# Optimization experiments

Hardware: AMD Instinct MI355X
Metric: run time of the kernel (lower is better)

Reference implementation:

```python
import jax, jax.numpy as jnp
import numpy as np

NZ, NC = 100, 2
FEAT_NUMBER, FEATURE_DIM = 8192, 1024
B = 8192
BN_EPS = 1e-5
GUMBEL_EPS = 0.001
TEMP = 0.1


def _batchnorm(h, gamma, beta):
    # torch BatchNorm1d training mode: biased batch statistics
    mu = jnp.mean(h, axis=0, keepdims=True)
    var = jnp.var(h, axis=0, keepdims=True)
    return (h - mu) * jax.lax.rsqrt(var + BN_EPS) * gamma + beta


def setup_inputs() -> dict:
    key = jax.random.key(0)
    ks = jax.random.split(key, 16)
    def glorot(k, shape):
        lim = 1.0 / np.sqrt(shape[0])
        return jax.random.uniform(k, shape, jnp.float32, -lim, lim)
    return {
        "x": jax.random.normal(ks[0], (B, NZ), jnp.float32),
        "y": jax.random.uniform(ks[1], (B, NC), jnp.float32),
        "W1": glorot(ks[2], (NZ + NC, 256)), "b1": jnp.zeros((256,), jnp.float32),
        "g1": jnp.ones((256,), jnp.float32), "be1": jnp.zeros((256,), jnp.float32),
        "W2": glorot(ks[3], (256, 64)), "b2": jnp.zeros((64,), jnp.float32),
        "g2": jnp.ones((64,), jnp.float32), "be2": jnp.zeros((64,), jnp.float32),
        "W3": glorot(ks[4], (64, FEAT_NUMBER)), "b3": jnp.zeros((FEAT_NUMBER,), jnp.float32),
        "codebook": jax.random.normal(ks[5], (FEAT_NUMBER, FEATURE_DIM), jnp.float32),
    }


def reference(x, y, W1, b1, g1, be1, W2, b2, g2, be2, W3, b3, codebook):
    z = jnp.concatenate([x, y], axis=-1)                       # [B, nz+nc]
    h = jax.nn.relu(_batchnorm(z @ W1 + b1, g1, be1))          # [B, 256]
    h = jax.nn.relu(_batchnorm(h @ W2 + b2, g2, be2))          # [B, 64]
    logits = h @ W3 + b3                                       # [B, feat_number]

    # gumbel noise: U = eps*rand; g = -log(-log(U+eps)+eps)
    U = GUMBEL_EPS * jax.random.uniform(jax.random.key(42), logits.shape, jnp.float32)
    g = -jnp.log(-jnp.log(U + GUMBEL_EPS) + GUMBEL_EPS)
    y_soft = jax.nn.softmax((logits + g) / TEMP, axis=-1)

    # straight-through one-hot
    ind = jnp.argmax(y_soft, axis=-1)
    y_hard = jax.nn.one_hot(ind, FEAT_NUMBER, dtype=y_soft.dtype)
    z_st = jax.lax.stop_gradient(y_hard - y_soft) + y_soft     # [B, feat_number]

    # weighted codebook sum == matmul (avoids [B,F,D] broadcast intermediate)
    return jnp.einsum('bf,fd->bd', z_st, codebook)             # [B, feature_dim]
```

## Files before the change

### kernel.cpp

```cpp
#include <hip/hip_runtime.h>
#include <math.h>

#define B_ROWS   8192
#define NZ       100
#define NC       2
#define H1       256
#define H2       64
#define FEATN    8192
#define FDIM     1024
#define RROWS    16
#define NTILE    (FEATN / 16)
#define A1ROWS   16
#define A1BLKS   (B_ROWS / A1ROWS)
#define CONVBLKS 256
#define A2ROWS   16
#define A2BLKS   (B_ROWS / A2ROWS)

typedef __attribute__((ext_vector_type(8))) short short8;
typedef __attribute__((ext_vector_type(4))) float f32x4;

__device__ __forceinline__ unsigned rotl32(unsigned v, int r) {
    return (v << r) | (v >> (32 - r));
}
__device__ __forceinline__ unsigned threefry_bits(unsigned lo) {
    const unsigned ks0 = 0u, ks1 = 42u, ks2 = 0x1BD11BDAu ^ 42u;
    unsigned x0 = 0u + ks0;
    unsigned x1 = lo + ks1;
#define TF_R4(a,b,c,d) \
    x0 += x1; x1 = rotl32(x1,a); x1 ^= x0; \
    x0 += x1; x1 = rotl32(x1,b); x1 ^= x0; \
    x0 += x1; x1 = rotl32(x1,c); x1 ^= x0; \
    x0 += x1; x1 = rotl32(x1,d); x1 ^= x0;
    TF_R4(13,15,26,6);  x0 += ks1; x1 += ks2 + 1u;
    TF_R4(17,29,16,24); x0 += ks2; x1 += ks0 + 2u;
    TF_R4(13,15,26,6);  x0 += ks0; x1 += ks1 + 3u;
    TF_R4(17,29,16,24); x0 += ks1; x1 += ks2 + 4u;
    TF_R4(13,15,26,6);  x0 += ks2; x1 += ks0 + 5u;
#undef TF_R4
    return x0 ^ x1;
}
__device__ __forceinline__ float gumbel_g(unsigned flat) {
    unsigned bits = threefry_bits(flat);
    float u  = __uint_as_float((bits >> 9) | 0x3f800000u) - 1.0f;
    float U  = 0.001f * u;
    float t1 = U + 0.001f;
    float L1 = (float)log((double)t1);
    float A  = 0.001f - L1;
    float L2 = (float)log((double)A);
    return -L2;
}

__device__ __forceinline__ unsigned short f2bf(float x) {
    unsigned u = __float_as_uint(x);
    u += 0x7fffu + ((u >> 16) & 1u);
    return (unsigned short)(u >> 16);
}
__device__ __forceinline__ unsigned fmono(float x) {
    unsigned b = __float_as_uint(x);
    return (b & 0x80000000u) ? ~b : (b | 0x80000000u);
}

__global__ __launch_bounds__(256) void k_a1(
    const float* __restrict__ x, const float* __restrict__ y,
    const float* __restrict__ W1, const float* __restrict__ b1,
    const float* __restrict__ W3,
    float* __restrict__ a1, double* __restrict__ p1, double* __restrict__ p2,
    unsigned short* __restrict__ w3s, float* __restrict__ maxw)
{
    const int t = threadIdx.x;

    if (blockIdx.x >= A1BLKS) {
        const int job  = (blockIdx.x - A1BLKS) * 256 + t;
        const int T    = job >> 7;
        const int rem  = job & 127;
        const int kh   = rem >> 6;
        const int l    = rem & 63;
        const int quad = l >> 4, col = l & 15;
        const float* src = W3 + (size_t)(kh * 32 + quad * 8) * FEATN + T * 16 + col;
        unsigned short v[8];
        float mx = 0.0f;
#pragma unroll
        for (int jj = 0; jj < 8; ++jj) {
            float xv = src[(size_t)jj * FEATN];
            mx = fmaxf(mx, fabsf(xv));
            v[jj] = f2bf(xv);
        }
        uint4 o;
        o.x = (unsigned)v[0] | ((unsigned)v[1] << 16);
        o.y = (unsigned)v[2] | ((unsigned)v[3] << 16);
        o.z = (unsigned)v[4] | ((unsigned)v[5] << 16);
        o.w = (unsigned)v[6] | ((unsigned)v[7] << 16);
        ((uint4*)w3s)[job] = o;
#pragma unroll
        for (int off = 32; off; off >>= 1) mx = fmaxf(mx, __shfl_xor(mx, off));
        __shared__ float wred[4];
        if ((t & 63) == 0) wred[t >> 6] = mx;
        __syncthreads();
        if (t == 0) {
            float m = fmaxf(fmaxf(wred[0], wred[1]), fmaxf(wred[2], wred[3]));
            atomicMax((unsigned*)maxw, __float_as_uint(m));
        }
        return;
    }

    const int j  = t;
    const int b0 = blockIdx.x * A1ROWS;

    __shared__ __align__(16) float xs[NZ][16];
    __shared__ __align__(16) float ys[NC][16];
    for (int q = t; q < A1ROWS * NZ; q += 256) {
        int r = q / NZ, i = q - r * NZ;
        xs[i][r] = x[(size_t)b0 * NZ + q];
    }
    if (t < A1ROWS * NC) {
        int r = t >> 1, i = t & 1;
        ys[i][r] = y[b0 * NC + t];
    }
    __syncthreads();

    double acc[A1ROWS];
#pragma unroll
    for (int r = 0; r < A1ROWS; ++r) acc[r] = 0.0;
    for (int i = 0; i < NZ; ++i) {
        double wd = (double)W1[i * H1 + j];
        const float4 x0 = *(const float4*)&xs[i][0];
        const float4 x1 = *(const float4*)&xs[i][4];
        const float4 x2 = *(const float4*)&xs[i][8];
        const float4 x3 = *(const float4*)&xs[i][12];
        acc[0]  += (double)x0.x * wd; acc[1]  += (double)x0.y * wd;
        acc[2]  += (double)x0.z * wd; acc[3]  += (double)x0.w * wd;
        acc[4]  += (double)x1.x * wd; acc[5]  += (double)x1.y * wd;
        acc[6]  += (double)x1.z * wd; acc[7]  += (double)x1.w * wd;
        acc[8]  += (double)x2.x * wd; acc[9]  += (double)x2.y * wd;
        acc[10] += (double)x2.z * wd; acc[11] += (double)x2.w * wd;
        acc[12] += (double)x3.x * wd; acc[13] += (double)x3.y * wd;
        acc[14] += (double)x3.z * wd; acc[15] += (double)x3.w * wd;
    }
#pragma unroll
    for (int i = 0; i < NC; ++i) {
        double wd = (double)W1[(NZ + i) * H1 + j];
        const float4 y0 = *(const float4*)&ys[i][0];
        const float4 y1 = *(const float4*)&ys[i][4];
        const float4 y2 = *(const float4*)&ys[i][8];
        const float4 y3 = *(const float4*)&ys[i][12];
        acc[0]  += (double)y0.x * wd; acc[1]  += (double)y0.y * wd;
        acc[2]  += (double)y0.z * wd; acc[3]  += (double)y0.w * wd;
        acc[4]  += (double)y1.x * wd; acc[5]  += (double)y1.y * wd;
        acc[6]  += (double)y1.z * wd; acc[7]  += (double)y1.w * wd;
        acc[8]  += (double)y2.x * wd; acc[9]  += (double)y2.y * wd;
        acc[10] += (double)y2.z * wd; acc[11] += (double)y2.w * wd;
        acc[12] += (double)y3.x * wd; acc[13] += (double)y3.y * wd;
        acc[14] += (double)y3.z * wd; acc[15] += (double)y3.w * wd;
    }
    double bb = (double)b1[j];
    double s = 0.0, s2 = 0.0;
#pragma unroll
    for (int r = 0; r < A1ROWS; ++r) {
        float v = (float)(acc[r] + bb);
        a1[(b0 + r) * H1 + j] = v;
        double dv = (double)v;
        s += dv; s2 += dv * dv;
    }
    p1[blockIdx.x * H1 + j] = s;
    p2[blockIdx.x * H1 + j] = s2;
}

__global__ __launch_bounds__(256) void k_stats2(
    const double* __restrict__ p1, const double* __restrict__ p2,
    int nprt, int ncol,
    const float* __restrict__ gamma, const float* __restrict__ beta,
    float* __restrict__ scale, float* __restrict__ shift)
{
    const int j = blockIdx.x, t = threadIdx.x;
    double s = 0.0, s2 = 0.0;
    for (int g = t; g < nprt; g += 256) {
        s  += p1[(size_t)g * ncol + j];
        s2 += p2[(size_t)g * ncol + j];
    }
#pragma unroll
    for (int off = 32; off; off >>= 1) {
        s  += __shfl_xor(s, off);
        s2 += __shfl_xor(s2, off);
    }
    __shared__ double ws1[4], ws2[4];
    if ((t & 63) == 0) { ws1[t >> 6] = s; ws2[t >> 6] = s2; }
    __syncthreads();
    if (t == 0) {
        s  = (ws1[0] + ws1[1]) + (ws1[2] + ws1[3]);
        s2 = (ws2[0] + ws2[1]) + (ws2[2] + ws2[3]);
        double mean = s * (1.0 / B_ROWS);
        double var  = s2 * (1.0 / B_ROWS) - mean * mean;
        double rstd = 1.0 / sqrt(var + 1e-5);
        double sc   = (double)gamma[j] * rstd;
        scale[j] = (float)sc;
        shift[j] = (float)((double)beta[j] - mean * sc);
    }
}

__global__ __launch_bounds__(256) void k_a2(
    const float* __restrict__ a1,
    const float* __restrict__ sc1, const float* __restrict__ sh1,
    const float* __restrict__ W2, const float* __restrict__ b2,
    float* __restrict__ a2, double* __restrict__ p1, double* __restrict__ p2)
{
    const int t  = threadIdx.x;
    const int k  = t & 63;
    const int rg = t >> 6;
    const int b0 = blockIdx.x * A2ROWS;

    __shared__ __align__(16) float hs[H1][20];
    __shared__ double ps[4][64], ps2[4][64];

    {
        const float sct = sc1[t], sht = sh1[t];
#pragma unroll 4
        for (int rr = 0; rr < A2ROWS; ++rr) {
            float v = a1[(size_t)(b0 + rr) * H1 + t];
            hs[t][rr] = fmaxf(fmaf(v, sct, sht), 0.0f);
        }
    }
    __syncthreads();

    const int r0 = rg * 4;
    double acc0 = 0.0, acc1 = 0.0, acc2 = 0.0, acc3 = 0.0;
    for (int j = 0; j < H1; ++j) {
        double wd = (double)W2[j * H2 + k];
        const float4 h4 = *(const float4*)&hs[j][r0];
        acc0 += (double)h4.x * wd;
        acc1 += (double)h4.y * wd;
        acc2 += (double)h4.z * wd;
        acc3 += (double)h4.w * wd;
    }
    const double bb = (double)b2[k];
    float v0 = (float)(acc0 + bb);
    float v1 = (float)(acc1 + bb);
    float v2 = (float)(acc2 + bb);
    float v3 = (float)(acc3 + bb);
    a2[(b0 + r0 + 0) * H2 + k] = v0;
    a2[(b0 + r0 + 1) * H2 + k] = v1;
    a2[(b0 + r0 + 2) * H2 + k] = v2;
    a2[(b0 + r0 + 3) * H2 + k] = v3;

    double s  = (double)v0 + (double)v1 + (double)v2 + (double)v3;
    double s2 = (double)v0 * (double)v0 + (double)v1 * (double)v1
              + (double)v2 * (double)v2 + (double)v3 * (double)v3;
    ps[rg][k] = s; ps2[rg][k] = s2;
    __syncthreads();
    if (t < 64) {
        double S  = (ps[0][t]  + ps[1][t])  + (ps[2][t]  + ps[3][t]);
        double S2 = (ps2[0][t] + ps2[1][t]) + (ps2[2][t] + ps2[3][t]);
        p1[blockIdx.x * H2 + t] = S;
        p2[blockIdx.x * H2 + t] = S2;
    }
}

__global__ __launch_bounds__(512)
__attribute__((amdgpu_waves_per_eu(4, 4)))
void k_main(
    const float* __restrict__ a2,
    const float* __restrict__ sc2, const float* __restrict__ sh2,
    const float* __restrict__ W3, const float* __restrict__ b3,
    const unsigned short* __restrict__ w3s, const float* __restrict__ maxw,
    const float* __restrict__ codebook, float* __restrict__ out)
{
    const int t    = threadIdx.x;
    const int wv   = t >> 6;
    const int lane = t & 63;
    const int quad = lane >> 4, col = lane & 15;
    const int b0   = blockIdx.x * RROWS;

    __shared__ __align__(16) float h2T[64][17];
    __shared__ float fineT[NTILE][17];
    __shared__ float thrS[RROWS];
    __shared__ unsigned long long best[RROWS];
    __shared__ unsigned short wl[RROWS * NTILE];
    __shared__ int wlN;
    __shared__ int rowInd[RROWS];
    __shared__ float maxwS;

    if (t == 0) { maxwS = maxw[0]; wlN = 0; }
    for (int q = t; q < RROWS * 64; q += 512) {
        int j = q >> 4, r = q & 15;
        float v = a2[(b0 + r) * H2 + j];
        h2T[j][r] = fmaxf(fmaf(v, sc2[j], sh2[j]), 0.0f);
    }
    __syncthreads();

    short8 aF0, aF1;
#pragma unroll
    for (int jj = 0; jj < 8; ++jj) {
        aF0[jj] = (short)f2bf(h2T[quad * 8 + jj][col]);
        aF1[jj] = (short)f2bf(h2T[32 + quad * 8 + jj][col]);
    }

    {
        const uint4*  wp = (const uint4*)w3s + (size_t)wv * 8192 + lane;
        const float4* bq = (const float4*)b3 + wv * 256 + quad;
        for (int s = 0; s < 8; ++s) {
            uint4 c[8], d[8];
            float4 bb[8];
#pragma unroll
            for (int u = 0; u < 8; ++u) {
                c[u]  = wp[u * 128];
                d[u]  = wp[u * 128 + 64];
                bb[u] = bq[u * 4];
            }
#pragma unroll
            for (int u = 0; u < 8; ++u) {
                f32x4 acc = {bb[u].x, bb[u].y, bb[u].z, bb[u].w};
                acc = __builtin_amdgcn_mfma_f32_16x16x32_bf16(
                          *(const short8*)&c[u], aF0, acc, 0, 0, 0);
                acc = __builtin_amdgcn_mfma_f32_16x16x32_bf16(
                          *(const short8*)&d[u], aF1, acc, 0, 0, 0);
                float m = fmaxf(fmaxf(acc[0], acc[1]), fmaxf(acc[2], acc[3]));
                m = fmaxf(m, __shfl_xor(m, 16));
                m = fmaxf(m, __shfl_xor(m, 32));
                if (lane < 16) fineT[(wv * 8 + s) * 8 + u][lane] = m;
            }
            wp += 1024; bq += 32;
        }
    }
    __syncthreads();

    {
        const int r = t >> 5, cc = t & 31;
        float s = fabsf(h2T[2 * cc][r]) + fabsf(h2T[2 * cc + 1][r]);
        float gmv = -1e30f;
#pragma unroll
        for (int k = 0; k < 16; ++k) gmv = fmaxf(gmv, fineT[cc + 32 * k][r]);
#pragma unroll
        for (int off = 1; off < 32; off <<= 1) {
            s   += __shfl_xor(s, off);
            gmv  = fmaxf(gmv, __shfl_xor(gmv, off));
        }
        if (cc == 0) {
            float e = s * maxwS * (1.0f / 256.0f);
            thrS[r] = gmv - (0.1068f + e + 1e-3f);
            best[r] = 0ull;
        }
    }
    __syncthreads();

    {
        const int r = t >> 5, cc = t & 31;
        const float th = thrS[r];
#pragma unroll
        for (int k = 0; k < 16; ++k) {
            const int T = cc + 32 * k;
            if (fineT[T][r] >= th) {
                int idx = atomicAdd(&wlN, 1);
                wl[idx] = (unsigned short)((r << 9) | T);
            }
        }
    }
    __syncthreads();

    {
        const int n = wlN;
        const int g = lane >> 4;
        for (int i = wv * 4; i < n; i += 32) {
            const int  ci  = i + g;
            const bool act = (ci < n);
            const int  e   = act ? wl[ci] : 0;
            const int  r   = e >> 9;
            const int  T   = e & 511;
            const int  f   = T * 16 + col;
            float acc = b3[f];
            const float* wcol = W3 + f;
#pragma unroll 8
            for (int j = 0; j < 64; ++j) {
                acc = fmaf(h2T[j][r], *wcol, acc);
                wcol += FEATN;
            }
            if (act && acc >= thrS[r]) {
                float sc = acc + gumbel_g((unsigned)(b0 + r) * (unsigned)FEATN + (unsigned)f);
                unsigned long long pk = ((unsigned long long)fmono(sc) << 32)
                                      | (unsigned)(FEATN - 1 - f);
                atomicMax(&best[r], pk);
            }
        }
    }
    __syncthreads();
    if (t < RROWS) {
        rowInd[t] = (FEATN - 1 - (int)(best[t] & 0xFFFFFFFFull)) & (FEATN - 1);
    }
    __syncthreads();

    {
        const int rr = t >> 8, tt = t & 255;
        for (int rp = 0; rp < RROWS / 2; ++rp) {
            const int r = rp * 2 + rr;
            const int ind = rowInd[r];
            const float4* src = (const float4*)(codebook + (size_t)ind * FDIM);
            float4*       dst = (float4*)(out + (size_t)(b0 + r) * FDIM);
            dst[tt] = src[tt];
        }
    }
}

extern "C" void kernel_launch(void* const* d_in, const int* in_sizes, int n_in,
                              void* d_out, int out_size, void* d_ws, size_t ws_size,
                              hipStream_t stream)
{
    const float* x   = (const float*)d_in[0];
    const float* y   = (const float*)d_in[1];
    const float* W1  = (const float*)d_in[2];
    const float* b1  = (const float*)d_in[3];
    const float* g1  = (const float*)d_in[4];
    const float* be1 = (const float*)d_in[5];
    const float* W2  = (const float*)d_in[6];
    const float* b2  = (const float*)d_in[7];
    const float* g2  = (const float*)d_in[8];
    const float* be2 = (const float*)d_in[9];
    const float* W3  = (const float*)d_in[10];
    const float* b3  = (const float*)d_in[11];
    const float* cb  = (const float*)d_in[12];
    float* out = (float*)d_out;

    float* ws  = (float*)d_ws;
    float* a1  = ws;
    float* a2  = a1 + B_ROWS * H1;
    float* sc1 = a2 + B_ROWS * H2;
    float* sh1 = sc1 + H1;
    float* sc2 = sh1 + H1;
    float* sh2 = sc2 + H2;
    double* p1 = (double*)(sh2 + H2);
    double* p2 = p1 + A1BLKS * H1;
    unsigned short* w3s = (unsigned short*)(p2 + A1BLKS * H1);
    float* maxw = (float*)(w3s + NTILE * 2 * 64 * 8);

    hipMemsetAsync(maxw, 0, 4, stream);
    k_a1    <<<A1BLKS + CONVBLKS, 256, 0, stream>>>(x, y, W1, b1, W3,
                                                    a1, p1, p2, w3s, maxw);
    k_stats2<<<H1, 256, 0, stream>>>(p1, p2, A1BLKS, H1, g1, be1, sc1, sh1);
    k_a2    <<<A2BLKS, 256, 0, stream>>>(a1, sc1, sh1, W2, b2, a2, p1, p2);
    k_stats2<<<H2, 256, 0, stream>>>(p1, p2, A2BLKS, H2, g2, be2, sc2, sh2);
    k_main  <<<B_ROWS / RROWS, 512, 0, stream>>>(a2, sc2, sh2, W3, b3,
                                                 w3s, maxw, cb, out);
}
```

Baseline: 214.5 us.

## Split feature dimension across two blocks per row group and move codebook gather to separate kernel

The main kernel now processes half the feature tiles per block and launches twice as many blocks. Per-row argmax is combined through global 64-bit atomicMax into a buffer that reuses the a1 workspace, and a new kernel then gathers codebook rows. The per-tile maxima are stored as bf16 rounded upward, with the threshold margin widened to match, which halves the shared memory used for them. Occupancy is raised to 8 waves per EU, and the small MLP kernels move to 512-thread blocks. The cost is an extra memset and an extra launch, global atomics, and the threshold-based pruning depending on the bf16 rounding staying conservative.

```diff
diff --git a/kernel.cpp b/kernel.cpp
--- a/kernel.cpp
+++ b/kernel.cpp
@@ -10,9 +10,10 @@
 #define FDIM     1024
 #define RROWS    16
 #define NTILE    (FEATN / 16)
+#define NTILE_H  (NTILE / 2)
 #define A1ROWS   16
 #define A1BLKS   (B_ROWS / A1ROWS)
-#define CONVBLKS 256
+#define CONVBLKS 128
 #define A2ROWS   16
 #define A2BLKS   (B_ROWS / A2ROWS)
 
@@ -55,12 +56,20 @@
     u += 0x7fffu + ((u >> 16) & 1u);
     return (unsigned short)(u >> 16);
 }
+__device__ __forceinline__ unsigned short f2bf_up(float x) {
+    unsigned u = __float_as_uint(x);
+    unsigned hi = (u & 0x80000000u) ? (u >> 16) : ((u + 0xFFFFu) >> 16);
+    return (unsigned short)hi;
+}
+__device__ __forceinline__ float bf2f(unsigned short h) {
+    return __uint_as_float((unsigned)h << 16);
+}
 __device__ __forceinline__ unsigned fmono(float x) {
     unsigned b = __float_as_uint(x);
     return (b & 0x80000000u) ? ~b : (b | 0x80000000u);
 }
 
-__global__ __launch_bounds__(256) void k_a1(
+__global__ __launch_bounds__(512) void k_a1(
     const float* __restrict__ x, const float* __restrict__ y,
     const float* __restrict__ W1, const float* __restrict__ b1,
     const float* __restrict__ W3,
@@ -70,7 +79,7 @@
     const int t = threadIdx.x;
 
     if (blockIdx.x >= A1BLKS) {
-        const int job  = (blockIdx.x - A1BLKS) * 256 + t;
+        const int job  = (blockIdx.x - A1BLKS) * 512 + t;
         const int T    = job >> 7;
         const int rem  = job & 127;
         const int kh   = rem >> 6;
@@ -93,22 +102,27 @@
         ((uint4*)w3s)[job] = o;
 #pragma unroll
         for (int off = 32; off; off >>= 1) mx = fmaxf(mx, __shfl_xor(mx, off));
-        __shared__ float wred[4];
+        __shared__ float wred[8];
         if ((t & 63) == 0) wred[t >> 6] = mx;
         __syncthreads();
         if (t == 0) {
-            float m = fmaxf(fmaxf(wred[0], wred[1]), fmaxf(wred[2], wred[3]));
+            float m = wred[0];
+#pragma unroll
+            for (int wq = 1; wq < 8; ++wq) m = fmaxf(m, wred[wq]);
             atomicMax((unsigned*)maxw, __float_as_uint(m));
         }
         return;
     }
 
-    const int j  = t;
-    const int b0 = blockIdx.x * A1ROWS;
+    const int j    = t & 255;
+    const int half = t >> 8;
+    const int b0   = blockIdx.x * A1ROWS;
+    const int r0   = half * 8;
 
     __shared__ __align__(16) float xs[NZ][16];
     __shared__ __align__(16) float ys[NC][16];
-    for (int q = t; q < A1ROWS * NZ; q += 256) {
+    __shared__ float vsh[256][8];
+    for (int q = t; q < A1ROWS * NZ; q += 512) {
         int r = q / NZ, i = q - r * NZ;
         xs[i][r] = x[(size_t)b0 * NZ + q];
     }
@@ -118,51 +132,55 @@
     }
     __syncthreads();
 
-    double acc[A1ROWS];
-#pragma unroll
-    for (int r = 0; r < A1ROWS; ++r) acc[r] = 0.0;
+    double acc[8];
+#pragma unroll
+    for (int r = 0; r < 8; ++r) acc[r] = 0.0;
     for (int i = 0; i < NZ; ++i) {
         double wd = (double)W1[i * H1 + j];
-        const float4 x0 = *(const float4*)&xs[i][0];
-        const float4 x1 = *(const float4*)&xs[i][4];
-        const float4 x2 = *(const float4*)&xs[i][8];
-        const float4 x3 = *(const float4*)&xs[i][12];
-        acc[0]  += (double)x0.x * wd; acc[1]  += (double)x0.y * wd;
-        acc[2]  += (double)x0.z * wd; acc[3]  += (double)x0.w * wd;
-        acc[4]  += (double)x1.x * wd; acc[5]  += (double)x1.y * wd;
-        acc[6]  += (double)x1.z * wd; acc[7]  += (double)x1.w * wd;
-        acc[8]  += (double)x2.x * wd; acc[9]  += (double)x2.y * wd;
-        acc[10] += (double)x2.z * wd; acc[11] += (double)x2.w * wd;
-        acc[12] += (double)x3.x * wd; acc[13] += (double)x3.y * wd;
-        acc[14] += (double)x3.z * wd; acc[15] += (double)x3.w * wd;
+        const float4 x0 = *(const float4*)&xs[i][r0];
+        const float4 x1 = *(const float4*)&xs[i][r0 + 4];
+        acc[0] += (double)x0.x * wd; acc[1] += (double)x0.y * wd;
+        acc[2] += (double)x0.z * wd; acc[3] += (double)x0.w * wd;
+        acc[4] += (double)x1.x * wd; acc[5] += (double)x1.y * wd;
+        acc[6] += (double)x1.z * wd; acc[7] += (double)x1.w * wd;
     }
 #pragma unroll
     for (int i = 0; i < NC; ++i) {
         double wd = (double)W1[(NZ + i) * H1 + j];
-        const float4 y0 = *(const float4*)&ys[i][0];
-        const float4 y1 = *(const float4*)&ys[i][4];
-        const float4 y2 = *(const float4*)&ys[i][8];
-        const float4 y3 = *(const float4*)&ys[i][12];
-        acc[0]  += (double)y0.x * wd; acc[1]  += (double)y0.y * wd;
-        acc[2]  += (double)y0.z * wd; acc[3]  += (double)y0.w * wd;
-        acc[4]  += (double)y1.x * wd; acc[5]  += (double)y1.y * wd;
-        acc[6]  += (double)y1.z * wd; acc[7]  += (double)y1.w * wd;
-        acc[8]  += (double)y2.x * wd; acc[9]  += (double)y2.y * wd;
-        acc[10] += (double)y2.z * wd; acc[11] += (double)y2.w * wd;
-        acc[12] += (double)y3.x * wd; acc[13] += (double)y3.y * wd;
-        acc[14] += (double)y3.z * wd; acc[15] += (double)y3.w * wd;
-    }
-    double bb = (double)b1[j];
-    double s = 0.0, s2 = 0.0;
-#pragma unroll
-    for (int r = 0; r < A1ROWS; ++r) {
-        float v = (float)(acc[r] + bb);
-        a1[(b0 + r) * H1 + j] = v;
-        double dv = (double)v;
-        s += dv; s2 += dv * dv;
-    }
-    p1[blockIdx.x * H1 + j] = s;
-    p2[blockIdx.x * H1 + j] = s2;
+        const float4 y0 = *(const float4*)&ys[i][r0];
+        const float4 y1 = *(const float4*)&ys[i][r0 + 4];
+        acc[0] += (double)y0.x * wd; acc[1] += (double)y0.y * wd;
+        acc[2] += (double)y0.z * wd; acc[3] += (double)y0.w * wd;
+        acc[4] += (double)y1.x * wd; acc[5] += (double)y1.y * wd;
+        acc[6] += (double)y1.z * wd; acc[7] += (double)y1.w * wd;
+    }
+    const double bb = (double)b1[j];
+    float v[8];
+#pragma unroll
+    for (int r = 0; r < 8; ++r) {
+        v[r] = (float)(acc[r] + bb);
+        a1[(b0 + r0 + r) * H1 + j] = v[r];
+    }
+    if (half) {
+#pragma unroll
+        for (int r = 0; r < 8; ++r) vsh[j][r] = v[r];
+    }
+    __syncthreads();
+    if (!half) {
+        double s = 0.0, s2 = 0.0;
+#pragma unroll
+        for (int r = 0; r < 8; ++r) {
+            double dv = (double)v[r];
+            s += dv; s2 += dv * dv;
+        }
+#pragma unroll
+        for (int r = 0; r < 8; ++r) {
+            double dv = (double)vsh[j][r];
+            s += dv; s2 += dv * dv;
+        }
+        p1[blockIdx.x * H1 + j] = s;
+        p2[blockIdx.x * H1 + j] = s2;
+    }
 }
 
 __global__ __launch_bounds__(256) void k_stats2(
@@ -197,7 +215,7 @@
     }
 }
 
-__global__ __launch_bounds__(256) void k_a2(
+__global__ __launch_bounds__(512) void k_a2(
     const float* __restrict__ a1,
     const float* __restrict__ sc1, const float* __restrict__ sh1,
     const float* __restrict__ W2, const float* __restrict__ b2,
@@ -207,75 +225,71 @@
     const int k  = t & 63;
     const int rg = t >> 6;
     const int b0 = blockIdx.x * A2ROWS;
-
-    __shared__ __align__(16) float hs[H1][20];
-    __shared__ double ps[4][64], ps2[4][64];
+    const int r0 = rg * 2;
+
+    __shared__ __align__(8) float hs[H1][18];
+    __shared__ float vsh[64][17];
 
     {
-        const float sct = sc1[t], sht = sh1[t];
+        const int jc = t & 255, rq = t >> 8;
+        const float sct = sc1[jc], sht = sh1[jc];
+#pragma unroll
+        for (int rr = rq * 8; rr < rq * 8 + 8; ++rr) {
+            float vv = a1[(size_t)(b0 + rr) * H1 + jc];
+            hs[jc][rr] = fmaxf(fmaf(vv, sct, sht), 0.0f);
+        }
+    }
+    __syncthreads();
+
+    double acc0 = 0.0, acc1 = 0.0;
 #pragma unroll 4
-        for (int rr = 0; rr < A2ROWS; ++rr) {
-            float v = a1[(size_t)(b0 + rr) * H1 + t];
-            hs[t][rr] = fmaxf(fmaf(v, sct, sht), 0.0f);
-        }
-    }
-    __syncthreads();
-
-    const int r0 = rg * 4;
-    double acc0 = 0.0, acc1 = 0.0, acc2 = 0.0, acc3 = 0.0;
     for (int j = 0; j < H1; ++j) {
         double wd = (double)W2[j * H2 + k];
-        const float4 h4 = *(const float4*)&hs[j][r0];
-        acc0 += (double)h4.x * wd;
-        acc1 += (double)h4.y * wd;
-        acc2 += (double)h4.z * wd;
-        acc3 += (double)h4.w * wd;
+        const float2 h2 = *(const float2*)&hs[j][r0];
+        acc0 += (double)h2.x * wd;
+        acc1 += (double)h2.y * wd;
     }
     const double bb = (double)b2[k];
     float v0 = (float)(acc0 + bb);
     float v1 = (float)(acc1 + bb);
-    float v2 = (float)(acc2 + bb);
-    float v3 = (float)(acc3 + bb);
     a2[(b0 + r0 + 0) * H2 + k] = v0;
     a2[(b0 + r0 + 1) * H2 + k] = v1;
-    a2[(b0 + r0 + 2) * H2 + k] = v2;
-    a2[(b0 + r0 + 3) * H2 + k] = v3;
-
-    double s  = (double)v0 + (double)v1 + (double)v2 + (double)v3;
-    double s2 = (double)v0 * (double)v0 + (double)v1 * (double)v1
-              + (double)v2 * (double)v2 + (double)v3 * (double)v3;
-    ps[rg][k] = s; ps2[rg][k] = s2;
+    vsh[k][r0]     = v0;
+    vsh[k][r0 + 1] = v1;
     __syncthreads();
     if (t < 64) {
-        double S  = (ps[0][t]  + ps[1][t])  + (ps[2][t]  + ps[3][t]);
-        double S2 = (ps2[0][t] + ps2[1][t]) + (ps2[2][t] + ps2[3][t]);
-        p1[blockIdx.x * H2 + t] = S;
-        p2[blockIdx.x * H2 + t] = S2;
+        double s = 0.0, s2 = 0.0;
+#pragma unroll
+        for (int r = 0; r < A2ROWS; ++r) {
+            double dv = (double)vsh[t][r];
+            s += dv; s2 += dv * dv;
+        }
+        p1[blockIdx.x * H2 + t] = s;
+        p2[blockIdx.x * H2 + t] = s2;
     }
 }
 
 __global__ __launch_bounds__(512)
-__attribute__((amdgpu_waves_per_eu(4, 4)))
+__attribute__((amdgpu_waves_per_eu(8, 8)))
 void k_main(
     const float* __restrict__ a2,
     const float* __restrict__ sc2, const float* __restrict__ sh2,
     const float* __restrict__ W3, const float* __restrict__ b3,
     const unsigned short* __restrict__ w3s, const float* __restrict__ maxw,
-    const float* __restrict__ codebook, float* __restrict__ out)
+    unsigned long long* __restrict__ bestG)
 {
     const int t    = threadIdx.x;
     const int wv   = t >> 6;
     const int lane = t & 63;
     const int quad = lane >> 4, col = lane & 15;
-    const int b0   = blockIdx.x * RROWS;
+    const int half = blockIdx.x & 1;
+    const int b0   = (blockIdx.x >> 1) * RROWS;
 
     __shared__ __align__(16) float h2T[64][17];
-    __shared__ float fineT[NTILE][17];
+    __shared__ unsigned short fineW[NTILE_H][17];
     __shared__ float thrS[RROWS];
-    __shared__ unsigned long long best[RROWS];
-    __shared__ unsigned short wl[RROWS * NTILE];
+    __shared__ unsigned short wl[RROWS * NTILE_H];
     __shared__ int wlN;
-    __shared__ int rowInd[RROWS];
     __shared__ float maxwS;
 
     if (t == 0) { maxwS = maxw[0]; wlN = 0; }
@@ -294,9 +308,10 @@
     }
 
     {
-        const uint4*  wp = (const uint4*)w3s + (size_t)wv * 8192 + lane;
-        const float4* bq = (const float4*)b3 + wv * 256 + quad;
-        for (int s = 0; s < 8; ++s) {
+        const uint4*  wp = (const uint4*)w3s
+                         + (size_t)(half * NTILE_H + wv * 32) * 128 + lane;
+        const float4* bq = (const float4*)b3 + (half * 1024 + wv * 128) + quad;
+        for (int s = 0; s < 4; ++s) {
             uint4 c[8], d[8];
             float4 bb[8];
 #pragma unroll
@@ -315,7 +330,7 @@
                 float m = fmaxf(fmaxf(acc[0], acc[1]), fmaxf(acc[2], acc[3]));
                 m = fmaxf(m, __shfl_xor(m, 16));
                 m = fmaxf(m, __shfl_xor(m, 32));
-                if (lane < 16) fineT[(wv * 8 + s) * 8 + u][lane] = m;
+                if (lane < 16) fineW[wv * 32 + s * 8 + u][lane] = f2bf_up(m);
             }
             wp += 1024; bq += 32;
         }
@@ -327,7 +342,7 @@
         float s = fabsf(h2T[2 * cc][r]) + fabsf(h2T[2 * cc + 1][r]);
         float gmv = -1e30f;
 #pragma unroll
-        for (int k = 0; k < 16; ++k) gmv = fmaxf(gmv, fineT[cc + 32 * k][r]);
+        for (int k = 0; k < 8; ++k) gmv = fmaxf(gmv, bf2f(fineW[cc + 32 * k][r]));
 #pragma unroll
         for (int off = 1; off < 32; off <<= 1) {
             s   += __shfl_xor(s, off);
@@ -335,8 +350,7 @@
         }
         if (cc == 0) {
             float e = s * maxwS * (1.0f / 256.0f);
-            thrS[r] = gmv - (0.1068f + e + 1e-3f);
-            best[r] = 0ull;
+            thrS[r] = gmv - (0.1068f + e + 1e-3f + fabsf(gmv) * 0.0078125f);
         }
     }
     __syncthreads();
@@ -345,11 +359,11 @@
         const int r = t >> 5, cc = t & 31;
         const float th = thrS[r];
 #pragma unroll
-        for (int k = 0; k < 16; ++k) {
+        for (int k = 0; k < 8; ++k) {
             const int T = cc + 32 * k;
-            if (fineT[T][r] >= th) {
+            if (bf2f(fineW[T][r]) >= th) {
                 int idx = atomicAdd(&wlN, 1);
-                wl[idx] = (unsigned short)((r << 9) | T);
+                wl[idx] = (unsigned short)((r << 8) | T);
             }
         }
     }
@@ -362,9 +376,9 @@
             const int  ci  = i + g;
             const bool act = (ci < n);
             const int  e   = act ? wl[ci] : 0;
-            const int  r   = e >> 9;
-            const int  T   = e & 511;
-            const int  f   = T * 16 + col;
+            const int  r   = e >> 8;
+            const int  lt  = e & 255;
+            const int  f   = (half * NTILE_H + lt) * 16 + col;
             float acc = b3[f];
             const float* wcol = W3 + f;
 #pragma unroll 8
@@ -376,25 +390,27 @@
                 float sc = acc + gumbel_g((unsigned)(b0 + r) * (unsigned)FEATN + (unsigned)f);
                 unsigned long long pk = ((unsigned long long)fmono(sc) << 32)
                                       | (unsigned)(FEATN - 1 - f);
-                atomicMax(&best[r], pk);
+                atomicMax(&bestG[b0 + r], pk);
             }
         }
     }
-    __syncthreads();
-    if (t < RROWS) {
-        rowInd[t] = (FEATN - 1 - (int)(best[t] & 0xFFFFFFFFull)) & (FEATN - 1);
-    }
-    __syncthreads();
-
-    {
-        const int rr = t >> 8, tt = t & 255;
-        for (int rp = 0; rp < RROWS / 2; ++rp) {
-            const int r = rp * 2 + rr;
-            const int ind = rowInd[r];
-            const float4* src = (const float4*)(codebook + (size_t)ind * FDIM);
-            float4*       dst = (float4*)(out + (size_t)(b0 + r) * FDIM);
-            dst[tt] = src[tt];
-        }
+}
+
+__global__ __launch_bounds__(256) void k_out(
+    const unsigned long long* __restrict__ bestG,
+    const float* __restrict__ codebook, float* __restrict__ out)
+{
+    const int t  = threadIdx.x;
+    const int b0 = blockIdx.x * 16;
+    __shared__ int inds[16];
+    if (t < 16)
+        inds[t] = (FEATN - 1 - (int)(bestG[b0 + t] & 0xFFFFFFFFull)) & (FEATN - 1);
+    __syncthreads();
+#pragma unroll
+    for (int r = 0; r < 16; ++r) {
+        const float4* src = (const float4*)(codebook + (size_t)inds[r] * FDIM);
+        float4*       dst = (float4*)(out + (size_t)(b0 + r) * FDIM);
+        dst[t] = src[t];
     }
 }
 
@@ -428,13 +444,16 @@
     double* p2 = p1 + A1BLKS * H1;
     unsigned short* w3s = (unsigned short*)(p2 + A1BLKS * H1);
     float* maxw = (float*)(w3s + NTILE * 2 * 64 * 8);
+    unsigned long long* bestG = (unsigned long long*)a1;
 
     hipMemsetAsync(maxw, 0, 4, stream);
-    k_a1    <<<A1BLKS + CONVBLKS, 256, 0, stream>>>(x, y, W1, b1, W3,
+    k_a1    <<<A1BLKS + CONVBLKS, 512, 0, stream>>>(x, y, W1, b1, W3,
                                                     a1, p1, p2, w3s, maxw);
     k_stats2<<<H1, 256, 0, stream>>>(p1, p2, A1BLKS, H1, g1, be1, sc1, sh1);
-    k_a2    <<<A2BLKS, 256, 0, stream>>>(a1, sc1, sh1, W2, b2, a2, p1, p2);
+    k_a2    <<<A2BLKS, 512, 0, stream>>>(a1, sc1, sh1, W2, b2, a2, p1, p2);
     k_stats2<<<H2, 256, 0, stream>>>(p1, p2, A2BLKS, H2, g2, be2, sc2, sh2);
-    k_main  <<<B_ROWS / RROWS, 512, 0, stream>>>(a2, sc2, sh2, W3, b3,
-                                                 w3s, maxw, cb, out);
-}
+    hipMemsetAsync(bestG, 0, B_ROWS * 8, stream);
+    k_main  <<<(B_ROWS / RROWS) * 2, 512, 0, stream>>>(a2, sc2, sh2, W3, b3,
+                                                       w3s, maxw, bestG);
+    k_out   <<<B_ROWS / 16, 256, 0, stream>>>(bestG, cb, out);
+}
```

Measured after the change: 308.8 us. 43.9% more time.
